# Kernel optimization log

Measured on AMD Instinct MI355X. Metric: run time of the kernel, lower is better.

Reference implementation:

```python
import jax, jax.numpy as jnp
import numpy as np

NUM_ITEM = 50000
D = 64
LN_EPS = 1e-5


def _l2norm(x, axis=-1):
    # F.normalize: x / max(||x||, eps)
    n = jnp.sqrt(jnp.sum(x * x, axis=axis, keepdims=True))
    return x / jnp.maximum(n, 1e-12)


def _mlp(x, w1, b1, w2, b2, w3, b3):
    h = jax.nn.relu(x @ w1.T + b1)
    h = jax.nn.relu(h @ w2.T + b2)
    return h @ w3.T + b3


def setup_inputs() -> dict:
    key = jax.random.key(0)
    ks = jax.random.split(key, 20)
    d_c, d_t = 1024, 768
    inp = {
        'seq_modify': jax.random.randint(ks[0], (1024, 50), 0, NUM_ITEM + 1),
        'content_feature': jax.random.normal(ks[1], (NUM_ITEM, d_c), jnp.float32),
        'text_feature': jax.random.normal(ks[2], (NUM_ITEM, d_t), jnp.float32),
        'cf_feature': jax.random.normal(ks[3], (NUM_ITEM, D), jnp.float32),
        'item_embeddings': jax.random.normal(ks[4], (NUM_ITEM, D), jnp.float32) * 0.05,
        'c_w1': jax.random.normal(ks[5], (d_c, d_c), jnp.float32) * (1.0 / np.sqrt(d_c)),
        'c_b1': jnp.zeros((d_c,), jnp.float32),
        'c_w2': jax.random.normal(ks[6], (256, d_c), jnp.float32) * (1.0 / np.sqrt(d_c)),
        'c_b2': jnp.zeros((256,), jnp.float32),
        'c_w3': jax.random.normal(ks[7], (D, 256), jnp.float32) * (1.0 / np.sqrt(256)),
        'c_b3': jnp.zeros((D,), jnp.float32),
        't_w1': jax.random.normal(ks[8], (d_t, d_t), jnp.float32) * (1.0 / np.sqrt(d_t)),
        't_b1': jnp.zeros((d_t,), jnp.float32),
        't_w2': jax.random.normal(ks[9], (256, d_t), jnp.float32) * (1.0 / np.sqrt(d_t)),
        't_b2': jnp.zeros((256,), jnp.float32),
        't_w3': jax.random.normal(ks[10], (D, 256), jnp.float32) * (1.0 / np.sqrt(256)),
        't_b3': jnp.zeros((D,), jnp.float32),
        'cf_w': jax.random.normal(ks[11], (D, D), jnp.float32) * (1.0 / np.sqrt(D)),
        'cf_b': jnp.zeros((D,), jnp.float32),
        'wq': jax.random.normal(ks[12], (D, D), jnp.float32) * (1.0 / np.sqrt(D)),
        'wk': jax.random.normal(ks[13], (D, D), jnp.float32) * (1.0 / np.sqrt(D)),
        'wv': jax.random.normal(ks[14], (D, D), jnp.float32) * (1.0 / np.sqrt(D)),
    }
    return inp


def reference(seq_modify, content_feature, text_feature, cf_feature, item_embeddings,
              c_w1, c_b1, c_w2, c_b2, c_w3, c_b3,
              t_w1, t_b1, t_w2, t_b2, t_w3, t_b3,
              cf_w, cf_b, wq, wk, wv):
    # padding index num_item -> 0 (masked_fill in torch forward)
    seq = jnp.where(seq_modify == NUM_ITEM, 0, seq_modify)  # [bs, n_token]

    # modality encoders over the full catalog (content/text L2-normalized in __init__)
    c_emb = _mlp(_l2norm(content_feature), c_w1, c_b1, c_w2, c_b2, c_w3, c_b3)  # [N, 64]
    t_emb = _mlp(_l2norm(text_feature), t_w1, t_b1, t_w2, t_b2, t_w3, t_b3)    # [N, 64]
    cf_emb = cf_feature @ cf_w.T + cf_b                                         # [N, 64]
    id_emb = item_embeddings                                                    # [N, 64]

    # gather per-token modality embeddings and stack modals: [bs, n, 4, 64]
    feats = jnp.stack([c_emb[seq], t_emb[seq], cf_emb[seq], id_emb[seq]], axis=-2)
    bs, n_tok, n_modal, d = feats.shape

    x = _l2norm(feats).reshape(-1, n_modal, d)  # [bs*n, 4, 64]

    # selfAttention: LayerNorm (no affine) -> q,k,v -> softmax attn -> mean pool
    mu = jnp.mean(x, axis=-1, keepdims=True)
    var = jnp.mean((x - mu) ** 2, axis=-1, keepdims=True)
    xn = (x - mu) / jnp.sqrt(var + LN_EPS)
    q = xn @ wq.T
    k = xn @ wk.T
    v = xn @ wv.T
    attn = jax.nn.softmax(jnp.einsum('bmd,bnd->bmn', q * (d ** -0.5), k), axis=-1)
    fused = jnp.einsum('bmn,bnd->bmd', attn, v).mean(axis=-2)  # [bs*n, 64]
    return fused.reshape(bs, n_tok, d)
```

## Files before the change

kernel.cpp:

```cpp
#include <hip/hip_runtime.h>
#include <hip/hip_bf16.h>
#include <type_traits>

typedef __hip_bfloat16 bf16;
typedef __attribute__((ext_vector_type(8))) short short8;
typedef __attribute__((ext_vector_type(4))) float floatx4;

static constexpr int kNumItem = 50000;

__device__ __forceinline__ float bf2f(const bf16 x) { return __bfloat162float(x); }

union alignas(16) Pack8 {
  bf16 b[8];
  short8 s;
};
union alignas(8) Pack4 {
  bf16 b[4];
  short4 s;
};

__device__ __forceinline__ void async_cp16(const void* g, void* l) {
  __builtin_amdgcn_global_load_lds((const __attribute__((address_space(1))) void*)g,
                                   (__attribute__((address_space(3))) void*)l, 16, 0, 0);
}

__device__ __forceinline__ int xcd_swz(int orig, int nwg) {
  const int nx = 8;
  const int q = nwg / nx, r = nwg % nx;
  const int xcd = orig % nx, loc = orig / nx;
  return (xcd < r ? xcd * (q + 1) : r * (q + 1) + (xcd - r) * q) + loc;
}

__global__ __launch_bounds__(256) void row_invnorm(const float* __restrict__ X,
                                                   float* __restrict__ out,
                                                   int M, int K) {
  const int lane = threadIdx.x & 63;
  const int wave = threadIdx.x >> 6;
  const int row = blockIdx.x * 4 + wave;
  if (row >= M) return;
  const float* xr = X + (size_t)row * K;
  float s = 0.f;
  for (int c = lane * 8; c < K; c += 64 * 8) {
    float4 a = *(const float4*)(xr + c);
    float4 b = *(const float4*)(xr + c + 4);
    s += a.x * a.x + a.y * a.y + a.z * a.z + a.w * a.w;
    s += b.x * b.x + b.y * b.y + b.z * b.z + b.w * b.w;
  }
#pragma unroll
  for (int off = 32; off > 0; off >>= 1) s += __shfl_xor(s, off, 64);
  if (lane == 0) out[row] = 1.0f / fmaxf(sqrtf(s), 1e-12f);
}

__global__ __launch_bounds__(256) void cvt_rows_norm(const float* __restrict__ X,
                                                     bf16* __restrict__ Xb,
                                                     float* __restrict__ out,
                                                     int M, int K) {
  const int lane = threadIdx.x & 63;
  const int wave = threadIdx.x >> 6;
  const int row = blockIdx.x * 4 + wave;
  if (row >= M) return;
  const float* xr = X + (size_t)row * K;
  bf16* dr = Xb + (size_t)row * K;
  float s = 0.f;
  for (int c = lane * 8; c < K; c += 64 * 8) {
    float4 a = *(const float4*)(xr + c);
    float4 b = *(const float4*)(xr + c + 4);
    s += a.x * a.x + a.y * a.y + a.z * a.z + a.w * a.w;
    s += b.x * b.x + b.y * b.y + b.z * b.z + b.w * b.w;
    Pack8 p;
    p.b[0] = __float2bfloat16(a.x); p.b[1] = __float2bfloat16(a.y);
    p.b[2] = __float2bfloat16(a.z); p.b[3] = __float2bfloat16(a.w);
    p.b[4] = __float2bfloat16(b.x); p.b[5] = __float2bfloat16(b.y);
    p.b[6] = __float2bfloat16(b.z); p.b[7] = __float2bfloat16(b.w);
    *(short8*)(void*)(dr + c) = p.s;
  }
#pragma unroll
  for (int off = 32; off > 0; off >>= 1) s += __shfl_xor(s, off, 64);
  if (lane == 0) out[row] = 1.0f / fmaxf(sqrtf(s), 1e-12f);
}

static constexpr int kNWSeg = 10;
struct WPack {
  const float* src[kNWSeg];
  int start4[kNWSeg];
  int total4;
};
__global__ __launch_bounds__(256) void cvt_many(WPack p, bf16* __restrict__ dst) {
  int c = blockIdx.x * 256 + threadIdx.x;
  const int stride = gridDim.x * 256;
  for (; c < p.total4; c += stride) {
    int s = 0;
#pragma unroll
    for (int k = 1; k < kNWSeg; k++)
      if (c >= p.start4[k]) s = k;
    const float4 v = ((const float4*)p.src[s])[c - p.start4[s]];
    Pack4 q;
    q.b[0] = __float2bfloat16(v.x); q.b[1] = __float2bfloat16(v.y);
    q.b[2] = __float2bfloat16(v.z); q.b[3] = __float2bfloat16(v.w);
    *(short4*)(void*)(dst + (size_t)c * 4) = q.s;
  }
}

template <int BM, int BN, typename AT, typename BT, typename CT>
__global__ __launch_bounds__(256) void gemm_bt(const AT* __restrict__ A,
                                               const BT* __restrict__ B,
                                               CT* __restrict__ C,
                                               int M, int N, int K,
                                               const float* __restrict__ rowScale,
                                               const float* __restrict__ bias,
                                               int doRelu) {
  constexpr int BK = 32;
  __shared__ __align__(16) bf16 sA[2][BM * BK];
  __shared__ __align__(16) bf16 sB[2][BN * BK];
  const int t = threadIdx.x;
  const int lane = t & 63;
  const int wave = t >> 6;
  constexpr int WN = BN / 64;
  const int wm = wave / WN;
  const int wn = wave % WN;
  const int gx = gridDim.x;
  const int wgid = xcd_swz(blockIdx.y * gx + blockIdx.x, gx * gridDim.y);
  const int m0 = (wgid / gx) * BM;
  const int n0 = (wgid % gx) * BN;
  const int lane16 = lane & 15;
  const int quad = lane >> 4;

  auto stageA = [&](int k0, bf16* dst) {
#pragma unroll
    for (int it = 0; it < BM / 64; ++it) {
      int c = t + 256 * it;
      int row = c >> 2;
      int col = (c & 3) * 8;
      int gr = m0 + row;
      if (gr > M - 1) gr = M - 1;
      if constexpr (std::is_same_v<AT, bf16>) {
        async_cp16(A + (size_t)gr * K + k0 + col, dst + c * 8);
      } else {
        const float* src = A + (size_t)gr * K + k0 + col;
        float4 fa = *(const float4*)src;
        float4 fb = *(const float4*)(src + 4);
        Pack8 p;
        p.b[0] = __float2bfloat16(fa.x); p.b[1] = __float2bfloat16(fa.y);
        p.b[2] = __float2bfloat16(fa.z); p.b[3] = __float2bfloat16(fa.w);
        p.b[4] = __float2bfloat16(fb.x); p.b[5] = __float2bfloat16(fb.y);
        p.b[6] = __float2bfloat16(fb.z); p.b[7] = __float2bfloat16(fb.w);
        *(short8*)(void*)(dst + c * 8) = p.s;
      }
    }
  };
  auto stageB = [&](int k0, bf16* dst) {
#pragma unroll
    for (int it = 0; it < BN / 64; ++it) {
      int c = t + 256 * it;
      int row = c >> 2;
      int col = (c & 3) * 8;
      int gr = n0 + row;
      if (gr > N - 1) gr = N - 1;
      if constexpr (std::is_same_v<BT, bf16>) {
        async_cp16(B + (size_t)gr * K + k0 + col, dst + c * 8);
      } else {
        const float* src = B + (size_t)gr * K + k0 + col;
        float4 fa = *(const float4*)src;
        float4 fb = *(const float4*)(src + 4);
        Pack8 p;
        p.b[0] = __float2bfloat16(fa.x); p.b[1] = __float2bfloat16(fa.y);
        p.b[2] = __float2bfloat16(fa.z); p.b[3] = __float2bfloat16(fa.w);
        p.b[4] = __float2bfloat16(fb.x); p.b[5] = __float2bfloat16(fb.y);
        p.b[6] = __float2bfloat16(fb.z); p.b[7] = __float2bfloat16(fb.w);
        *(short8*)(void*)(dst + c * 8) = p.s;
      }
    }
  };

  floatx4 acc[4][4];
#pragma unroll
  for (int i = 0; i < 4; i++)
#pragma unroll
    for (int j = 0; j < 4; j++) acc[i][j] = (floatx4)0.0f;

  stageA(0, sA[0]);
  stageB(0, sB[0]);
  __syncthreads();
  int cur = 0;
  for (int k0 = 0; k0 < K; k0 += BK) {
    const int nxt = cur ^ 1;
    if (k0 + BK < K) {
      stageA(k0 + BK, sA[nxt]);
      stageB(k0 + BK, sB[nxt]);
    }
    short8 afr[4], bfr[4];
#pragma unroll
    for (int i = 0; i < 4; i++)
      afr[i] = *(const short8*)(const void*)&sA[cur][(wm * 64 + i * 16 + lane16) * BK + quad * 8];
#pragma unroll
    for (int j = 0; j < 4; j++)
      bfr[j] = *(const short8*)(const void*)&sB[cur][(wn * 64 + j * 16 + lane16) * BK + quad * 8];
#pragma unroll
    for (int i = 0; i < 4; i++)
#pragma unroll
      for (int j = 0; j < 4; j++)
        acc[i][j] = __builtin_amdgcn_mfma_f32_16x16x32_bf16(afr[i], bfr[j], acc[i][j], 0, 0, 0);
    __syncthreads();
    cur = nxt;
  }

#pragma unroll
  for (int i = 0; i < 4; i++) {
#pragma unroll
    for (int j = 0; j < 4; j++) {
      const int col = n0 + wn * 64 + j * 16 + lane16;
      const float bv = bias ? bias[col] : 0.f;
#pragma unroll
      for (int r = 0; r < 4; r++) {
        const int row = m0 + wm * 64 + i * 16 + quad * 4 + r;
        if (row < M) {
          float v = acc[i][j][r];
          if (rowScale) v *= rowScale[row];
          v += bv;
          if (doRelu) v = v > 0.f ? v : 0.f;
          if constexpr (std::is_same_v<CT, bf16>)
            C[(size_t)row * N + col] = __float2bfloat16(v);
          else
            C[(size_t)row * N + col] = v;
        }
      }
    }
  }
}

template <typename CT>
__global__ __launch_bounds__(512) void gemm_bt2(const bf16* __restrict__ A,
                                                const bf16* __restrict__ B,
                                                CT* __restrict__ C,
                                                int M, int N, int K,
                                                const float* __restrict__ rowScale,
                                                const float* __restrict__ bias,
                                                int doRelu) {
  constexpr int BM = 128, BN = 256, BK = 32;
  __shared__ __align__(16) bf16 sA[2][BM * BK];
  __shared__ __align__(16) bf16 sB[2][BN * BK];
  const int t = threadIdx.x;
  const int lane = t & 63;
  const int wave = t >> 6;
  const int wm = wave >> 2;
  const int wn = wave & 3;
  const int gx = gridDim.x;
  const int wgid = xcd_swz(blockIdx.y * gx + blockIdx.x, gx * gridDim.y);
  const int m0 = (wgid / gx) * BM;
  const int n0 = (wgid % gx) * BN;
  const int lane16 = lane & 15;
  const int quad = lane >> 4;

  auto stage = [&](int k0, bf16* dA, bf16* dB) {
    {
      const int c = t;
      const int row = c >> 2;
      const int col = (c & 3) * 8;
      int gr = m0 + row;
      if (gr > M - 1) gr = M - 1;
      async_cp16(A + (size_t)gr * K + k0 + col, dA + c * 8);
    }
#pragma unroll
    for (int it = 0; it < 2; ++it) {
      const int c = t + 512 * it;
      const int row = c >> 2;
      const int col = (c & 3) * 8;
      int gr = n0 + row;
      if (gr > N - 1) gr = N - 1;
      async_cp16(B + (size_t)gr * K + k0 + col, dB + c * 8);
    }
  };

  floatx4 acc[4][4];
#pragma unroll
  for (int i = 0; i < 4; i++)
#pragma unroll
    for (int j = 0; j < 4; j++) acc[i][j] = (floatx4)0.0f;

  stage(0, sA[0], sB[0]);
  __syncthreads();
  int cur = 0;
  for (int k0 = 0; k0 < K; k0 += BK) {
    const int nxt = cur ^ 1;
    if (k0 + BK < K) stage(k0 + BK, sA[nxt], sB[nxt]);

    short8 afr[4], bfr[4];
#pragma unroll
    for (int i = 0; i < 4; i++)
      afr[i] = *(const short8*)(const void*)&sA[cur][(wm * 64 + i * 16 + lane16) * BK + quad * 8];
#pragma unroll
    for (int j = 0; j < 4; j++)
      bfr[j] = *(const short8*)(const void*)&sB[cur][(wn * 64 + j * 16 + lane16) * BK + quad * 8];
#pragma unroll
    for (int i = 0; i < 4; i++)
#pragma unroll
      for (int j = 0; j < 4; j++)
        acc[i][j] = __builtin_amdgcn_mfma_f32_16x16x32_bf16(afr[i], bfr[j], acc[i][j], 0, 0, 0);
    __syncthreads();
    cur = nxt;
  }

#pragma unroll
  for (int i = 0; i < 4; i++) {
#pragma unroll
    for (int j = 0; j < 4; j++) {
      const int col = n0 + wn * 64 + j * 16 + lane16;
      const float bv = bias ? bias[col] : 0.f;
#pragma unroll
      for (int r = 0; r < 4; r++) {
        const int row = m0 + wm * 64 + i * 16 + quad * 4 + r;
        if (row < M) {
          float v = acc[i][j][r];
          if (rowScale) v *= rowScale[row];
          v += bv;
          if (doRelu) v = v > 0.f ? v : 0.f;
          if constexpr (std::is_same_v<CT, bf16>)
            C[(size_t)row * N + col] = __float2bfloat16(v);
          else
            C[(size_t)row * N + col] = v;
        }
      }
    }
  }
}

__global__ __launch_bounds__(256) void norm_ln(const bf16* __restrict__ c_emb,
                                               const bf16* __restrict__ t_emb,
                                               const bf16* __restrict__ cf_emb,
                                               const float* __restrict__ id_emb,
                                               bf16* __restrict__ Xn, int nItem) {
  const int gid = blockIdx.x * 256 + threadIdx.x;
  const int row = gid >> 4;
  const int d4 = gid & 15;
  if (row >= nItem * 4) return;
  const int item = row >> 2;
  const int m = row & 3;

  float x[4];
  if (m == 3) {
    const float4 f = *(const float4*)(id_emb + (size_t)item * 64 + d4 * 4);
    x[0] = f.x; x[1] = f.y; x[2] = f.z; x[3] = f.w;
  } else {
    const bf16* src = (m == 0) ? c_emb : (m == 1 ? t_emb : cf_emb);
    Pack4 p;
    p.s = *(const short4*)(const void*)(src + (size_t)item * 64 + d4 * 4);
    x[0] = bf2f(p.b[0]); x[1] = bf2f(p.b[1]); x[2] = bf2f(p.b[2]); x[3] = bf2f(p.b[3]);
  }

  float sm = x[0] + x[1] + x[2] + x[3];
  float ss = x[0] * x[0] + x[1] * x[1] + x[2] * x[2] + x[3] * x[3];
#pragma unroll
  for (int off = 1; off < 16; off <<= 1) {
    sm += __shfl_xor(sm, off, 64);
    ss += __shfl_xor(ss, off, 64);
  }
  const float inv = 1.0f / fmaxf(sqrtf(ss), 1e-12f);
  const float mu = sm * inv * (1.0f / 64.0f);
  const float ex2 = ss * inv * inv * (1.0f / 64.0f);
  const float var = ex2 - mu * mu;
  const float rs = rsqrtf(var + 1e-5f);

  Pack4 o;
#pragma unroll
  for (int c = 0; c < 4; c++) o.b[c] = __float2bfloat16((x[c] * inv - mu) * rs);
  *(short4*)(void*)(Xn + (size_t)row * 64 + d4 * 4) = o.s;
}

__global__ __launch_bounds__(256) void attn4(const bf16* __restrict__ QK,
                                             const float* __restrict__ V,
                                             float* __restrict__ out, int nGroup) {
  const int t = threadIdx.x;
  const int wave = t >> 6;
  const int lane = t & 63;
  const int sub = lane >> 4;
  const int d4 = lane & 15;
  const int group = blockIdx.x * 4 + wave;
  if (group >= nGroup) return;
  const int item = group * 4 + sub;
  const size_t rb = (size_t)item * 4;

  float4 q4[4], k4[4], v4[4];
#pragma unroll
  for (int m = 0; m < 4; m++) {
    Pack4 pq, pk;
    pq.s = *(const short4*)(const void*)(QK + (rb + m) * 128 + d4 * 4);
    pk.s = *(const short4*)(const void*)(QK + (rb + m) * 128 + 64 + d4 * 4);
    q4[m] = float4{bf2f(pq.b[0]), bf2f(pq.b[1]), bf2f(pq.b[2]), bf2f(pq.b[3])};
    k4[m] = float4{bf2f(pk.b[0]), bf2f(pk.b[1]), bf2f(pk.b[2]), bf2f(pk.b[3])};
    v4[m] = *(const float4*)(V + (rb + m) * 64 + d4 * 4);
  }

  float p[16];
#pragma unroll
  for (int m = 0; m < 4; m++)
#pragma unroll
    for (int n = 0; n < 4; n++)
      p[m * 4 + n] = q4[m].x * k4[n].x + q4[m].y * k4[n].y +
                     q4[m].z * k4[n].z + q4[m].w * k4[n].w;
#pragma unroll
  for (int off = 1; off < 16; off <<= 1)
#pragma unroll
    for (int i = 0; i < 16; i++) p[i] += __shfl_xor(p[i], off, 64);

  float abar[4] = {0, 0, 0, 0};
#pragma unroll
  for (int m = 0; m < 4; m++) {
    const float s0 = p[m * 4 + 0] * 0.125f, s1 = p[m * 4 + 1] * 0.125f;
    const float s2 = p[m * 4 + 2] * 0.125f, s3 = p[m * 4 + 3] * 0.125f;
    const float mx = fmaxf(fmaxf(s0, s1), fmaxf(s2, s3));
    const float e0 = expf(s0 - mx), e1 = expf(s1 - mx);
    const float e2 = expf(s2 - mx), e3 = expf(s3 - mx);
    const float inv = 1.0f / (e0 + e1 + e2 + e3);
    abar[0] += e0 * inv;
    abar[1] += e1 * inv;
    abar[2] += e2 * inv;
    abar[3] += e3 * inv;
  }

  float4 o;
  o.x = 0.25f * (abar[0] * v4[0].x + abar[1] * v4[1].x + abar[2] * v4[2].x + abar[3] * v4[3].x);
  o.y = 0.25f * (abar[0] * v4[0].y + abar[1] * v4[1].y + abar[2] * v4[2].y + abar[3] * v4[3].y);
  o.z = 0.25f * (abar[0] * v4[0].z + abar[1] * v4[1].z + abar[2] * v4[2].z + abar[3] * v4[3].z);
  o.w = 0.25f * (abar[0] * v4[0].w + abar[1] * v4[1].w + abar[2] * v4[2].w + abar[3] * v4[3].w);
  *(float4*)(out + (size_t)item * 64 + d4 * 4) = o;
}

__global__ __launch_bounds__(256, 4) void fuse_attn2(const int* __restrict__ seq,
                                                     const bf16* __restrict__ c_emb,
                                                     const bf16* __restrict__ t_emb,
                                                     const bf16* __restrict__ cf_emb,
                                                     const float* __restrict__ id_emb,
                                                     const float* __restrict__ wq,
                                                     const float* __restrict__ wk,
                                                     const float* __restrict__ wv,
                                                     float* __restrict__ out, int n_tok) {
  __shared__ __align__(16) float4 swc[3072];
  __shared__ float sxn[4][4][64];
  const int t = threadIdx.x;
  const int lane = t & 63;
  const int wave = t >> 6;

  for (int c = t; c < 3072; c += 256) {
    const int mat = c >> 10, rem = c & 1023, d4 = rem >> 6, j = rem & 63;
    const float* W = (mat == 0) ? wq : (mat == 1 ? wk : wv);
    swc[c] = *(const float4*)(W + j * 64 + d4 * 4);
  }
  __syncthreads();

  const int gw = blockIdx.x * 4 + wave;
  const int gstride = gridDim.x * 4;
  for (int token = gw; token < n_tok; token += gstride) {
    int idx = seq ? seq[token] : token;
    if (idx >= kNumItem || idx < 0) idx = 0;

    float x[4];
    x[0] = bf2f(c_emb[(size_t)idx * 64 + lane]);
    x[1] = bf2f(t_emb[(size_t)idx * 64 + lane]);
    x[2] = bf2f(cf_emb[(size_t)idx * 64 + lane]);
    x[3] = id_emb[(size_t)idx * 64 + lane];

#pragma unroll
    for (int m = 0; m < 4; m++) {
      float sm = x[m], ss = x[m] * x[m];
#pragma unroll
      for (int off = 32; off > 0; off >>= 1) {
        sm += __shfl_xor(sm, off, 64);
        ss += __shfl_xor(ss, off, 64);
      }
      const float inv = 1.0f / fmaxf(sqrtf(ss), 1e-12f);
      const float xh = x[m] * inv;
      const float mu = sm * inv * (1.0f / 64.0f);
      const float ex2 = ss * inv * inv * (1.0f / 64.0f);
      const float var = ex2 - mu * mu;
      const float xn = (xh - mu) * rsqrtf(var + 1e-5f);
      x[m] = xn;
      sxn[wave][m][lane] = xn;
    }

    float q[4] = {0, 0, 0, 0}, kk[4] = {0, 0, 0, 0}, v[4] = {0, 0, 0, 0};
#pragma unroll
    for (int d4 = 0; d4 < 16; d4++) {
      const float4 a = swc[d4 * 64 + lane];
      const float4 b = swc[1024 + d4 * 64 + lane];
      const float4 g = swc[2048 + d4 * 64 + lane];
#pragma unroll
      for (int m = 0; m < 4; m++) {
        const float4 xn4 = *(const float4*)&sxn[wave][m][d4 * 4];
        q[m] += xn4.x * a.x + xn4.y * a.y + xn4.z * a.z + xn4.w * a.w;
        kk[m] += xn4.x * b.x + xn4.y * b.y + xn4.z * b.z + xn4.w * b.w;
        v[m] += xn4.x * g.x + xn4.y * g.y + xn4.z * g.z + xn4.w * g.w;
      }
    }

    float p[16];
#pragma unroll
    for (int m = 0; m < 4; m++)
#pragma unroll
      for (int n = 0; n < 4; n++) p[m * 4 + n] = q[m] * kk[n];
#pragma unroll
    for (int off = 1; off < 64; off <<= 1)
#pragma unroll
      for (int i = 0; i < 16; i++) p[i] += __shfl_xor(p[i], off, 64);

    float abar[4] = {0, 0, 0, 0};
#pragma unroll
    for (int m = 0; m < 4; m++) {
      float s0 = p[m * 4 + 0] * 0.125f, s1 = p[m * 4 + 1] * 0.125f;
      float s2 = p[m * 4 + 2] * 0.125f, s3 = p[m * 4 + 3] * 0.125f;
      float mx = fmaxf(fmaxf(s0, s1), fmaxf(s2, s3));
      float e0 = expf(s0 - mx), e1 = expf(s1 - mx), e2 = expf(s2 - mx), e3 = expf(s3 - mx);
      float inv = 1.0f / (e0 + e1 + e2 + e3);
      abar[0] += e0 * inv;
      abar[1] += e1 * inv;
      abar[2] += e2 * inv;
      abar[3] += e3 * inv;
    }
    const float o =
        0.25f * (abar[0] * v[0] + abar[1] * v[1] + abar[2] * v[2] + abar[3] * v[3]);
    out[(size_t)token * 64 + lane] = o;
  }
}

__global__ __launch_bounds__(256) void gather_out(const int* __restrict__ seq,
                                                  const float* __restrict__ fused,
                                                  float* __restrict__ out, int n_tok) {
  const int gid = blockIdx.x * 256 + threadIdx.x;
  if (gid >= n_tok * 16) return;
  const int token = gid >> 4;
  const int c4 = gid & 15;
  int idx = seq[token];
  if (idx >= kNumItem || idx < 0) idx = 0;
  ((float4*)out)[(size_t)token * 16 + c4] = ((const float4*)fused)[(size_t)idx * 16 + c4];
}

extern "C" void kernel_launch(void* const* d_in, const int* in_sizes, int n_in,
                              void* d_out, int out_size, void* d_ws, size_t ws_size,
                              hipStream_t stream) {
  const int* seq = (const int*)d_in[0];
  const float* content = (const float*)d_in[1];
  const float* text = (const float*)d_in[2];
  const float* cf_feat = (const float*)d_in[3];
  const float* item_emb = (const float*)d_in[4];
  const float* c_w1 = (const float*)d_in[5];
  const float* c_b1 = (const float*)d_in[6];
  const float* c_w2 = (const float*)d_in[7];
  const float* c_b2 = (const float*)d_in[8];
  const float* c_w3 = (const float*)d_in[9];
  const float* c_b3 = (const float*)d_in[10];
  const float* t_w1 = (const float*)d_in[11];
  const float* t_b1 = (const float*)d_in[12];
  const float* t_w2 = (const float*)d_in[13];
  const float* t_b2 = (const float*)d_in[14];
  const float* t_w3 = (const float*)d_in[15];
  const float* t_b3 = (const float*)d_in[16];
  const float* cf_w = (const float*)d_in[17];
  const float* cf_b = (const float*)d_in[18];
  const float* wq = (const float*)d_in[19];
  const float* wk = (const float*)d_in[20];
  const float* wv = (const float*)d_in[21];
  float* out = (float*)d_out;

  const int M = kNumItem;
  const int n_tok = in_sizes[0];

  char* w = (char*)d_ws;
  size_t off = 0;
  auto alloc = [&](size_t bytes) -> void* {
    void* p = w + off;
    off += (bytes + 255) & ~(size_t)255;
    return p;
  };
  float* invn_c = (float*)alloc((size_t)M * 4);
  float* invn_t = (float*)alloc((size_t)M * 4);
  bf16* c_emb = (bf16*)alloc((size_t)M * 64 * 2);
  bf16* t_emb = (bf16*)alloc((size_t)M * 64 * 2);
  bf16* cf_emb = (bf16*)alloc((size_t)M * 64 * 2);
  bf16* H1 = (bf16*)alloc((size_t)M * 1024 * 2);
  bf16* H2 = (bf16*)alloc((size_t)M * 256 * 2);

  const int nw[kNWSeg] = {1024 * 1024, 256 * 1024, 64 * 256, 768 * 768, 256 * 768,
                          64 * 256,    64 * 64,    64 * 64,  64 * 64,   64 * 64};
  int wofs[kNWSeg + 1];
  wofs[0] = 0;
  for (int i = 0; i < kNWSeg; i++) wofs[i + 1] = wofs[i] + nw[i];
  bf16* Wb = (bf16*)alloc((size_t)wofs[kNWSeg] * 2);
  const bool useWb = (off <= ws_size);
  bf16* Ab = (bf16*)alloc((size_t)M * 1024 * 2);
  const bool useAb = useWb && (off <= ws_size);
  float* fusedTab = (float*)alloc((size_t)M * 64 * 4);
  const bool useFused = (off <= ws_size);

  const int R = M * 4;
  bf16* Xn = (bf16*)Ab;
  float* Vbuf = (float*)((char*)Ab + (size_t)R * 64 * 2);
  bf16* QKbuf = (bf16*)H1;

  if (useWb) {
    WPack p;
    const float* srcs[kNWSeg] = {c_w1, c_w2, c_w3, t_w1, t_w2, t_w3, cf_w, wq, wk, wv};
    for (int i = 0; i < kNWSeg; i++) {
      p.src[i] = srcs[i];
      p.start4[i] = wofs[i] / 4;
    }
    p.total4 = wofs[kNWSeg] / 4;
    cvt_many<<<dim3(2048), dim3(256), 0, stream>>>(p, Wb);
  }

  if (useAb) {
    cvt_rows_norm<<<dim3((M + 3) / 4), dim3(256), 0, stream>>>(content, Ab, invn_c, M, 1024);
    gemm_bt2<bf16><<<dim3(1024 / 256, (M + 127) / 128), dim3(512), 0, stream>>>(
        Ab, Wb + wofs[0], H1, M, 1024, 1024, invn_c, c_b1, 1);
    gemm_bt2<bf16><<<dim3(1, (M + 127) / 128), dim3(512), 0, stream>>>(
        H1, Wb + wofs[1], H2, M, 256, 1024, nullptr, c_b2, 1);
    gemm_bt<256, 64, bf16, bf16, bf16>
        <<<dim3(1, (M + 255) / 256), dim3(256), 0, stream>>>(
            H2, Wb + wofs[2], c_emb, M, 64, 256, nullptr, c_b3, 0);

    cvt_rows_norm<<<dim3((M + 3) / 4), dim3(256), 0, stream>>>(text, Ab, invn_t, M, 768);
    gemm_bt2<bf16><<<dim3(768 / 256, (M + 127) / 128), dim3(512), 0, stream>>>(
        Ab, Wb + wofs[3], H1, M, 768, 768, invn_t, t_b1, 1);
    gemm_bt2<bf16><<<dim3(1, (M + 127) / 128), dim3(512), 0, stream>>>(
        H1, Wb + wofs[4], H2, M, 256, 768, nullptr, t_b2, 1);
    gemm_bt<256, 64, bf16, bf16, bf16>
        <<<dim3(1, (M + 255) / 256), dim3(256), 0, stream>>>(
            H2, Wb + wofs[5], t_emb, M, 64, 256, nullptr, t_b3, 0);

    gemm_bt<256, 64, float, bf16, bf16>
        <<<dim3(1, (M + 255) / 256), dim3(256), 0, stream>>>(
            cf_feat, Wb + wofs[6], cf_emb, M, 64, 64, nullptr, cf_b, 0);

    norm_ln<<<dim3((R * 16 + 255) / 256), dim3(256), 0, stream>>>(
        c_emb, t_emb, cf_emb, item_emb, Xn, M);
    gemm_bt<256, 64, bf16, bf16, bf16>
        <<<dim3(2, (R + 255) / 256), dim3(256), 0, stream>>>(
            Xn, Wb + wofs[7], QKbuf, R, 128, 64, nullptr, nullptr, 0);
    gemm_bt<256, 64, bf16, bf16, float>
        <<<dim3(1, (R + 255) / 256), dim3(256), 0, stream>>>(
            Xn, Wb + wofs[9], Vbuf, R, 64, 64, nullptr, nullptr, 0);
    const int nGroup = (M + 3) / 4;
    attn4<<<dim3((nGroup + 3) / 4), dim3(256), 0, stream>>>(
        QKbuf, Vbuf, fusedTab, nGroup);
    gather_out<<<dim3((n_tok * 16 + 255) / 256), dim3(256), 0, stream>>>(
        seq, fusedTab, out, n_tok);
  } else if (useWb) {
    row_invnorm<<<dim3((M + 3) / 4), dim3(256), 0, stream>>>(content, invn_c, M, 1024);
    row_invnorm<<<dim3((M + 3) / 4), dim3(256), 0, stream>>>(text, invn_t, M, 768);
    gemm_bt<128, 128, float, bf16, bf16>
        <<<dim3(1024 / 128, (M + 127) / 128), dim3(256), 0, stream>>>(
            content, Wb + wofs[0], H1, M, 1024, 1024, invn_c, c_b1, 1);
    gemm_bt<128, 128, bf16, bf16, bf16>
        <<<dim3(256 / 128, (M + 127) / 128), dim3(256), 0, stream>>>(
            H1, Wb + wofs[1], H2, M, 256, 1024, nullptr, c_b2, 1);
    gemm_bt<256, 64, bf16, bf16, bf16>
        <<<dim3(1, (M + 255) / 256), dim3(256), 0, stream>>>(
            H2, Wb + wofs[2], c_emb, M, 64, 256, nullptr, c_b3, 0);
    gemm_bt<128, 128, float, bf16, bf16>
        <<<dim3(768 / 128, (M + 127) / 128), dim3(256), 0, stream>>>(
            text, Wb + wofs[3], H1, M, 768, 768, invn_t, t_b1, 1);
    gemm_bt<128, 128, bf16, bf16, bf16>
        <<<dim3(256 / 128, (M + 127) / 128), dim3(256), 0, stream>>>(
            H1, Wb + wofs[4], H2, M, 256, 768, nullptr, t_b2, 1);
    gemm_bt<256, 64, bf16, bf16, bf16>
        <<<dim3(1, (M + 255) / 256), dim3(256), 0, stream>>>(
            H2, Wb + wofs[5], t_emb, M, 64, 256, nullptr, t_b3, 0);
    gemm_bt<256, 64, float, bf16, bf16>
        <<<dim3(1, (M + 255) / 256), dim3(256), 0, stream>>>(
            cf_feat, Wb + wofs[6], cf_emb, M, 64, 64, nullptr, cf_b, 0);
    if (useFused) {
      fuse_attn2<<<dim3(768), dim3(256), 0, stream>>>(
          nullptr, c_emb, t_emb, cf_emb, item_emb, wq, wk, wv, fusedTab, M);
      gather_out<<<dim3((n_tok * 16 + 255) / 256), dim3(256), 0, stream>>>(
          seq, fusedTab, out, n_tok);
    } else {
      fuse_attn2<<<dim3(768), dim3(256), 0, stream>>>(
          seq, c_emb, t_emb, cf_emb, item_emb, wq, wk, wv, out, n_tok);
    }
  } else {
    row_invnorm<<<dim3((M + 3) / 4), dim3(256), 0, stream>>>(content, invn_c, M, 1024);
    row_invnorm<<<dim3((M + 3) / 4), dim3(256), 0, stream>>>(text, invn_t, M, 768);
    gemm_bt<128, 128, float, float, bf16>
        <<<dim3(1024 / 128, (M + 127) / 128), dim3(256), 0, stream>>>(
            content, c_w1, H1, M, 1024, 1024, invn_c, c_b1, 1);
    gemm_bt<128, 128, bf16, float, bf16>
        <<<dim3(256 / 128, (M + 127) / 128), dim3(256), 0, stream>>>(
            H1, c_w2, H2, M, 256, 1024, nullptr, c_b2, 1);
    gemm_bt<256, 64, bf16, float, bf16>
        <<<dim3(1, (M + 255) / 256), dim3(256), 0, stream>>>(
            H2, c_w3, c_emb, M, 64, 256, nullptr, c_b3, 0);
    gemm_bt<128, 128, float, float, bf16>
        <<<dim3(768 / 128, (M + 127) / 128), dim3(256), 0, stream>>>(
            text, t_w1, H1, M, 768, 768, invn_t, t_b1, 1);
    gemm_bt<128, 128, bf16, float, bf16>
        <<<dim3(256 / 128, (M + 127) / 128), dim3(256), 0, stream>>>(
            H1, t_w2, H2, M, 256, 768, nullptr, t_b2, 1);
    gemm_bt<256, 64, bf16, float, bf16>
        <<<dim3(1, (M + 255) / 256), dim3(256), 0, stream>>>(
            H2, t_w3, t_emb, M, 64, 256, nullptr, t_b3, 0);
    gemm_bt<256, 64, float, float, bf16>
        <<<dim3(1, (M + 255) / 256), dim3(256), 0, stream>>>(
            cf_feat, cf_w, cf_emb, M, 64, 64, nullptr, cf_b, 0);
    fuse_attn2<<<dim3(768), dim3(256), 0, stream>>>(
        seq, c_emb, t_emb, cf_emb, item_emb, wq, wk, wv, out, n_tok);
  }
}
```

Before: 999.0 us.

## Use fine-grained vmcnt waits to keep two async LDS stages in flight

Reworks the GEMM main loops so two K-tiles are issued ahead through async global-to-LDS loads. Each iteration waits only on the older tile's vmcnt rather than a full __syncthreads drain, and refills the buffer just consumed. The aim is to overlap memory latency with MFMA work more deeply and to stop draining all outstanding loads each step. It relies on exact vmcnt counts matching the number of loads each stage issues, so a wrong count could cause data races.

```diff
diff --git a/kernel.cpp b/kernel.cpp
--- a/kernel.cpp
+++ b/kernel.cpp
@@ -22,6 +22,23 @@
 __device__ __forceinline__ void async_cp16(const void* g, void* l) {
   __builtin_amdgcn_global_load_lds((const __attribute__((address_space(1))) void*)g,
                                    (__attribute__((address_space(3))) void*)l, 16, 0, 0);
+}
+
+template <int N>
+__device__ __forceinline__ void wait_vm() {
+  static_assert(N >= 0 && N <= 8, "unsupported vmcnt");
+  if constexpr (N == 0) asm volatile("s_waitcnt vmcnt(0)" ::: "memory");
+  else if constexpr (N == 1) asm volatile("s_waitcnt vmcnt(1)" ::: "memory");
+  else if constexpr (N == 2) asm volatile("s_waitcnt vmcnt(2)" ::: "memory");
+  else if constexpr (N == 3) asm volatile("s_waitcnt vmcnt(3)" ::: "memory");
+  else if constexpr (N == 4) asm volatile("s_waitcnt vmcnt(4)" ::: "memory");
+  else if constexpr (N == 5) asm volatile("s_waitcnt vmcnt(5)" ::: "memory");
+  else if constexpr (N == 6) asm volatile("s_waitcnt vmcnt(6)" ::: "memory");
+  else if constexpr (N == 7) asm volatile("s_waitcnt vmcnt(7)" ::: "memory");
+  else asm volatile("s_waitcnt vmcnt(8)" ::: "memory");
+}
+__device__ __forceinline__ void wait_lgkm0() {
+  asm volatile("s_waitcnt lgkmcnt(0)" ::: "memory");
 }
 
 __device__ __forceinline__ int xcd_swz(int orig, int nwg) {
@@ -178,30 +195,69 @@
 #pragma unroll
     for (int j = 0; j < 4; j++) acc[i][j] = (floatx4)0.0f;
 
-  stageA(0, sA[0]);
-  stageB(0, sB[0]);
-  __syncthreads();
-  int cur = 0;
-  for (int k0 = 0; k0 < K; k0 += BK) {
-    const int nxt = cur ^ 1;
-    if (k0 + BK < K) {
-      stageA(k0 + BK, sA[nxt]);
-      stageB(k0 + BK, sB[nxt]);
-    }
-    short8 afr[4], bfr[4];
-#pragma unroll
-    for (int i = 0; i < 4; i++)
-      afr[i] = *(const short8*)(const void*)&sA[cur][(wm * 64 + i * 16 + lane16) * BK + quad * 8];
-#pragma unroll
-    for (int j = 0; j < 4; j++)
-      bfr[j] = *(const short8*)(const void*)&sB[cur][(wn * 64 + j * 16 + lane16) * BK + quad * 8];
-#pragma unroll
-    for (int i = 0; i < 4; i++)
+  if constexpr (std::is_same_v<AT, bf16> && std::is_same_v<BT, bf16>) {
+    constexpr int LPT = BM / 64 + BN / 64;
+    const int nt = K / BK;
+    stageA(0, sA[0]);
+    stageB(0, sB[0]);
+    if (nt > 1) {
+      stageA(BK, sA[1]);
+      stageB(BK, sB[1]);
+    }
+    for (int tt = 0; tt < nt; ++tt) {
+      const int cur = tt & 1;
+      if (tt + 1 < nt) wait_vm<LPT>();
+      else wait_vm<0>();
+      __builtin_amdgcn_sched_barrier(0);
+      __builtin_amdgcn_s_barrier();
+
+      short8 afr[4], bfr[4];
+#pragma unroll
+      for (int i = 0; i < 4; i++)
+        afr[i] = *(const short8*)(const void*)&sA[cur][(wm * 64 + i * 16 + lane16) * BK + quad * 8];
 #pragma unroll
       for (int j = 0; j < 4; j++)
-        acc[i][j] = __builtin_amdgcn_mfma_f32_16x16x32_bf16(afr[i], bfr[j], acc[i][j], 0, 0, 0);
+        bfr[j] = *(const short8*)(const void*)&sB[cur][(wn * 64 + j * 16 + lane16) * BK + quad * 8];
+#pragma unroll
+      for (int i = 0; i < 4; i++)
+#pragma unroll
+        for (int j = 0; j < 4; j++)
+          acc[i][j] = __builtin_amdgcn_mfma_f32_16x16x32_bf16(afr[i], bfr[j], acc[i][j], 0, 0, 0);
+
+      wait_lgkm0();
+      __builtin_amdgcn_sched_barrier(0);
+      __builtin_amdgcn_s_barrier();
+      if (tt + 2 < nt) {
+        stageA((tt + 2) * BK, sA[cur]);
+        stageB((tt + 2) * BK, sB[cur]);
+      }
+    }
+  } else {
+    stageA(0, sA[0]);
+    stageB(0, sB[0]);
     __syncthreads();
-    cur = nxt;
+    int cur = 0;
+    for (int k0 = 0; k0 < K; k0 += BK) {
+      const int nxt = cur ^ 1;
+      if (k0 + BK < K) {
+        stageA(k0 + BK, sA[nxt]);
+        stageB(k0 + BK, sB[nxt]);
+      }
+      short8 afr[4], bfr[4];
+#pragma unroll
+      for (int i = 0; i < 4; i++)
+        afr[i] = *(const short8*)(const void*)&sA[cur][(wm * 64 + i * 16 + lane16) * BK + quad * 8];
+#pragma unroll
+      for (int j = 0; j < 4; j++)
+        bfr[j] = *(const short8*)(const void*)&sB[cur][(wn * 64 + j * 16 + lane16) * BK + quad * 8];
+#pragma unroll
+      for (int i = 0; i < 4; i++)
+#pragma unroll
+        for (int j = 0; j < 4; j++)
+          acc[i][j] = __builtin_amdgcn_mfma_f32_16x16x32_bf16(afr[i], bfr[j], acc[i][j], 0, 0, 0);
+      __syncthreads();
+      cur = nxt;
+    }
   }
 
 #pragma unroll
@@ -277,12 +333,15 @@
 #pragma unroll
     for (int j = 0; j < 4; j++) acc[i][j] = (floatx4)0.0f;
 
+  const int nt = K / BK;
   stage(0, sA[0], sB[0]);
-  __syncthreads();
-  int cur = 0;
-  for (int k0 = 0; k0 < K; k0 += BK) {
-    const int nxt = cur ^ 1;
-    if (k0 + BK < K) stage(k0 + BK, sA[nxt], sB[nxt]);
+  if (nt > 1) stage(BK, sA[1], sB[1]);
+  for (int tt = 0; tt < nt; ++tt) {
+    const int cur = tt & 1;
+    if (tt + 1 < nt) wait_vm<3>();
+    else wait_vm<0>();
+    __builtin_amdgcn_sched_barrier(0);
+    __builtin_amdgcn_s_barrier();
 
     short8 afr[4], bfr[4];
 #pragma unroll
@@ -296,8 +355,11 @@
 #pragma unroll
       for (int j = 0; j < 4; j++)
         acc[i][j] = __builtin_amdgcn_mfma_f32_16x16x32_bf16(afr[i], bfr[j], acc[i][j], 0, 0, 0);
-    __syncthreads();
-    cur = nxt;
+
+    wait_lgkm0();
+    __builtin_amdgcn_sched_barrier(0);
+    __builtin_amdgcn_s_barrier();
+    if (tt + 2 < nt) stage((tt + 2) * BK, sA[cur], sB[cur]);
   }
 
 #pragma unroll
```

New measurement: 987.6 us. About the same (-1.1%).
